# Optimization experiments

Hardware: AMD Instinct MI355X
Metric: run time of the kernel (lower is better)

## Reference

```python
import jax, jax.numpy as jnp
import numpy as np

B, N, DIN, DOUT, H = 4, 2048, 256, 256, 4
HD = DOUT // H
NEG_SLOPE = 0.2


def setup_inputs() -> dict:
    key = jax.random.key(0)
    k1, k2, k3, k4, k5 = jax.random.split(key, 5)
    x = jax.random.normal(k1, (B, N, DIN), dtype=jnp.float32)
    adj = jax.random.randint(k2, (B, N, N), 0, 2).astype(jnp.float32)
    # ensure self-loops so every softmax row has at least one valid entry
    adj = jnp.maximum(adj, jnp.eye(N, dtype=jnp.float32)[None])
    # xavier-uniform-ish scales
    w_bound = float(np.sqrt(6.0 / (DIN + DOUT)))
    a_bound = float(np.sqrt(6.0 / (1 + HD)))
    W = jax.random.uniform(k3, (DOUT, DIN), jnp.float32, -w_bound, w_bound)
    a_src = jax.random.uniform(k4, (H, HD), jnp.float32, -a_bound, a_bound)
    a_dst = jax.random.uniform(k5, (H, HD), jnp.float32, -a_bound, a_bound)
    return {"x": x, "adj": adj, "W": W, "a_src": a_src, "a_dst": a_dst}


def reference(x, adj, W, a_src, a_dst):
    b, n, _ = x.shape
    h = (x @ W.T).reshape(b, n, H, HD)                      # [B,N,H,HD]
    s_src = jnp.einsum('bnhd,hd->bnh', h, a_src)            # [B,N,H]
    s_dst = jnp.einsum('bnhd,hd->bnh', h, a_dst)            # [B,N,H]
    # e[b,i,j,h] = leaky_relu(s_src[b,i,h] + s_dst[b,j,h])
    e = jax.nn.leaky_relu(s_src[:, :, None, :] + s_dst[:, None, :, :], NEG_SLOPE)
    e = jnp.where(adj[..., None] == 0, -jnp.inf, e)         # [B,N,N,H]
    alpha = jax.nn.softmax(e, axis=2)                       # softmax over j (dropout is identity at eval)
    out = jnp.einsum('bijh,bjhd->bihd', alpha, h)           # weighted aggregate
    return out.reshape(b, n, DOUT)
```

## Files before the change

### kernel.cpp

```cpp
#include <hip/hip_runtime.h>
#include <math.h>

#define Bb   4
#define Nn   2048
#define Dd   256
#define Hh   4
#define HDd  64
#define BN   (Bb * Nn)

typedef float v4f __attribute__((ext_vector_type(4)));
typedef short v8s __attribute__((ext_vector_type(8)));

__device__ __forceinline__ unsigned rne_bf16(float f) {
    unsigned u = __float_as_uint(f);
    u += 0x7fffu + ((u >> 16) & 1u);
    return u >> 16;
}

__global__ __launch_bounds__(256, 2) void k_gemm(const float* __restrict__ x,
                                                 const float* __restrict__ W,
                                                 const float* __restrict__ a_src,
                                                 const float* __restrict__ a_dst,
                                                 unsigned short* __restrict__ hbf,
                                                 float* __restrict__ ssrc,
                                                 float* __restrict__ sdst) {
    __shared__ __align__(16) unsigned short xs[2][64 * 72];
    __shared__ __align__(16) unsigned short wsm[2][64 * 72];
    __shared__ float asd[128];

    const int tid = threadIdx.x;
    const int m0 = (int)(blockIdx.x >> 2) * 64;
    const int head = (int)blockIdx.x & 3;
    const int n0 = head * 64;
    const int b = m0 >> 11;
    const int i0loc = m0 & 2047;

    if (tid < 128) {
        int sel = tid >> 6, d = tid & 63;
        asd[tid] = sel ? a_dst[n0 + d] : a_src[n0 + d];
    }

    const int wv = tid >> 6, ln = tid & 63, l15 = ln & 15, l4 = ln >> 4;
    const int mh = wv >> 1, nh = wv & 1;
    const int srow = tid >> 2, kq = (tid & 3) * 16;

    v4f acc[2][2];
#pragma unroll
    for (int g = 0; g < 2; ++g)
#pragma unroll
        for (int t = 0; t < 2; ++t) acc[g][t] = (v4f){0.f, 0.f, 0.f, 0.f};

    for (int st = 0; st < 4; ++st) {
        const int k0 = st * 64;
        __syncthreads();
        {
            float xf[16], wf[16];
            const float* xp = x + (size_t)(m0 + srow) * Dd + k0 + kq;
            const float* wp = W + (size_t)(n0 + srow) * Dd + k0 + kq;
#pragma unroll
            for (int q = 0; q < 4; ++q) {
                *(float4*)&xf[q * 4] = *(const float4*)(xp + q * 4);
                *(float4*)&wf[q * 4] = *(const float4*)(wp + q * 4);
            }
            unsigned xh[8], xl[8], wh[8], wl[8];
#pragma unroll
            for (int j = 0; j < 8; ++j) {
                unsigned h0 = rne_bf16(xf[2 * j]), h1 = rne_bf16(xf[2 * j + 1]);
                float l0 = xf[2 * j] - __uint_as_float(h0 << 16);
                float l1 = xf[2 * j + 1] - __uint_as_float(h1 << 16);
                xh[j] = h0 | (h1 << 16);
                xl[j] = rne_bf16(l0) | (rne_bf16(l1) << 16);
                unsigned g0 = rne_bf16(wf[2 * j]), g1 = rne_bf16(wf[2 * j + 1]);
                float m0f = wf[2 * j] - __uint_as_float(g0 << 16);
                float m1f = wf[2 * j + 1] - __uint_as_float(g1 << 16);
                wh[j] = g0 | (g1 << 16);
                wl[j] = rne_bf16(m0f) | (rne_bf16(m1f) << 16);
            }
            *(uint4*)(xs[0] + srow * 72 + kq)     = make_uint4(xh[0], xh[1], xh[2], xh[3]);
            *(uint4*)(xs[0] + srow * 72 + kq + 8) = make_uint4(xh[4], xh[5], xh[6], xh[7]);
            *(uint4*)(xs[1] + srow * 72 + kq)     = make_uint4(xl[0], xl[1], xl[2], xl[3]);
            *(uint4*)(xs[1] + srow * 72 + kq + 8) = make_uint4(xl[4], xl[5], xl[6], xl[7]);
            *(uint4*)(wsm[0] + srow * 72 + kq)     = make_uint4(wh[0], wh[1], wh[2], wh[3]);
            *(uint4*)(wsm[0] + srow * 72 + kq + 8) = make_uint4(wh[4], wh[5], wh[6], wh[7]);
            *(uint4*)(wsm[1] + srow * 72 + kq)     = make_uint4(wl[0], wl[1], wl[2], wl[3]);
            *(uint4*)(wsm[1] + srow * 72 + kq + 8) = make_uint4(wl[4], wl[5], wl[6], wl[7]);
        }
        __syncthreads();
        {
            v8s ah[2][2], al[2][2], bh_[2][2], bl_[2][2];
#pragma unroll
            for (int g = 0; g < 2; ++g)
#pragma unroll
                for (int kh = 0; kh < 2; ++kh) {
                    int ro = (mh * 32 + g * 16 + l15) * 72 + kh * 32 + l4 * 8;
                    ah[g][kh] = *(const v8s*)(xs[0] + ro);
                    al[g][kh] = *(const v8s*)(xs[1] + ro);
                }
#pragma unroll
            for (int t = 0; t < 2; ++t)
#pragma unroll
                for (int kh = 0; kh < 2; ++kh) {
                    int ro = (nh * 32 + t * 16 + l15) * 72 + kh * 32 + l4 * 8;
                    bh_[t][kh] = *(const v8s*)(wsm[0] + ro);
                    bl_[t][kh] = *(const v8s*)(wsm[1] + ro);
                }
#pragma unroll
            for (int g = 0; g < 2; ++g)
#pragma unroll
                for (int t = 0; t < 2; ++t)
#pragma unroll
                    for (int kh = 0; kh < 2; ++kh) {
                        acc[g][t] = __builtin_amdgcn_mfma_f32_16x16x32_bf16(ah[g][kh], bh_[t][kh], acc[g][t], 0, 0, 0);
                        acc[g][t] = __builtin_amdgcn_mfma_f32_16x16x32_bf16(al[g][kh], bh_[t][kh], acc[g][t], 0, 0, 0);
                        acc[g][t] = __builtin_amdgcn_mfma_f32_16x16x32_bf16(ah[g][kh], bl_[t][kh], acc[g][t], 0, 0, 0);
                    }
        }
    }

    __syncthreads();
    float* T = (float*)&xs[0][0];
#pragma unroll
    for (int g = 0; g < 2; ++g)
#pragma unroll
        for (int t = 0; t < 2; ++t)
#pragma unroll
            for (int r = 0; r < 4; ++r) {
                int d = nh * 32 + t * 16 + l15;
                int m = mh * 32 + g * 16 + l4 * 4 + r;
                T[d * 67 + m] = acc[g][t][r];
            }
    __syncthreads();
    if (tid < 128) {
        int m = tid & 63, sel = tid >> 6;
        float s = 0.f;
#pragma unroll
        for (int d = 0; d < 64; ++d) s += T[d * 67 + m] * asd[sel * 64 + d];
        (sel ? sdst : ssrc)[(size_t)head * BN + (size_t)b * Nn + i0loc + m] = s;
        int dloc = tid >> 1, jh = tid & 1;
        const float* row = T + dloc * 67 + jh * 32;
        unsigned pk[16];
#pragma unroll
        for (int jj = 0; jj < 16; ++jj)
            pk[jj] = rne_bf16(row[jj * 2]) | (rne_bf16(row[jj * 2 + 1]) << 16);
        unsigned short* dst = hbf +
            ((size_t)((b * 64 + (i0loc >> 5) + jh) * 256 + head * HDd + dloc)) * 32;
        uint4* d4 = (uint4*)dst;
        d4[0] = make_uint4(pk[0], pk[1], pk[2], pk[3]);
        d4[1] = make_uint4(pk[4], pk[5], pk[6], pk[7]);
        d4[2] = make_uint4(pk[8], pk[9], pk[10], pk[11]);
        d4[3] = make_uint4(pk[12], pk[13], pk[14], pk[15]);
    }
}

__global__ __launch_bounds__(512, 4) void k_aggr(const unsigned short* __restrict__ hbf,
                                                 const float* __restrict__ adj,
                                                 const float* __restrict__ ssrc,
                                                 const float* __restrict__ sdst,
                                                 float* __restrict__ out) {
    __shared__ __align__(16) unsigned short Aw[2][64 * 72];

    const int tid = threadIdx.x;
    const int bid = (int)blockIdx.x;
    const int hp  = (bid >> 3) & 1;
    const int lin = (bid & 7) | ((bid >> 4) << 3);
    const int b  = lin >> 6;
    const int i0 = (lin & 63) * 32;

    const int gi = tid >> 4, jq = tid & 15;
    const int wv = tid >> 6;
    const int hl = wv >> 2, tl = wv & 3;
    const int ln = tid & 63, l15 = ln & 15, l4 = ln >> 4;

    const float ss0 = ssrc[(size_t)(hp * 2 + 0) * BN + (size_t)b * Nn + i0 + gi];
    const float ss1 = ssrc[(size_t)(hp * 2 + 1) * BN + (size_t)b * Nn + i0 + gi];
    const float* adjr = adj + (size_t)b * Nn * Nn + (size_t)(i0 + gi) * Nn;
    const float* sdr0 = sdst + (size_t)(hp * 2 + 0) * BN + (size_t)b * Nn;
    const float* sdr1 = sdst + (size_t)(hp * 2 + 1) * BN + (size_t)b * Nn;

    const unsigned short* hrow = hbf +
        ((size_t)b * 64 * 256 + (size_t)(hp * 128 + hl * 64 + tl * 16 + l15)) * 32 + l4 * 8;

    const v8s ones = {0x3F80, 0x3F80, 0x3F80, 0x3F80, 0x3F80, 0x3F80, 0x3F80, 0x3F80};

    v4f acc[2], zac[2];
#pragma unroll
    for (int g = 0; g < 2; ++g) {
        acc[g] = (v4f){0.f, 0.f, 0.f, 0.f};
        zac[g] = (v4f){0.f, 0.f, 0.f, 0.f};
    }

    float4 ajv = *(const float4*)(adjr + jq * 4);
    float4 sda = *(const float4*)(sdr0 + jq * 4);
    float4 sdb = *(const float4*)(sdr1 + jq * 4);

    for (int st = 0; st < 32; ++st) {
        {
            const float adjv[4] = {ajv.x, ajv.y, ajv.z, ajv.w};
            const float sa[4] = {sda.x, sda.y, sda.z, sda.w};
            const float sb[4] = {sdb.x, sdb.y, sdb.z, sdb.w};
            unsigned pk0[2], pk1[2];
#pragma unroll
            for (int k = 0; k < 4; ++k) {
                float e0 = ss0 + sa[k];
                float e1 = ss1 + sb[k];
                e0 = fmaxf(e0, 0.2f * e0);
                e1 = fmaxf(e1, 0.2f * e1);
                unsigned u0 = rne_bf16(adjv[k] * __expf(e0));
                unsigned u1 = rne_bf16(adjv[k] * __expf(e1));
                if (k & 1) { pk0[k >> 1] |= u0 << 16; pk1[k >> 1] |= u1 << 16; }
                else       { pk0[k >> 1] = u0;        pk1[k >> 1] = u1; }
            }
            *(uint2*)(Aw[st & 1] + gi * 72 + jq * 4)        = make_uint2(pk0[0], pk0[1]);
            *(uint2*)(Aw[st & 1] + (32 + gi) * 72 + jq * 4) = make_uint2(pk1[0], pk1[1]);
        }
        __syncthreads();
        {
            const int jn = ((st + 1) & 31) * 64;
            ajv = *(const float4*)(adjr + jn + jq * 4);
            sda = *(const float4*)(sdr0 + jn + jq * 4);
            sdb = *(const float4*)(sdr1 + jn + jq * 4);
        }
        {
            const unsigned short* awp = Aw[st & 1];
            v8s b0 = *(const v8s*)(hrow + (size_t)(2 * st + 0) * 8192);
            v8s b1 = *(const v8s*)(hrow + (size_t)(2 * st + 1) * 8192);
            v8s a00 = *(const v8s*)(awp + (hl * 32 + l15) * 72 + l4 * 8);
            v8s a01 = *(const v8s*)(awp + (hl * 32 + l15) * 72 + 32 + l4 * 8);
            v8s a10 = *(const v8s*)(awp + (hl * 32 + 16 + l15) * 72 + l4 * 8);
            v8s a11 = *(const v8s*)(awp + (hl * 32 + 16 + l15) * 72 + 32 + l4 * 8);
            acc[0] = __builtin_amdgcn_mfma_f32_16x16x32_bf16(a00, b0, acc[0], 0, 0, 0);
            acc[0] = __builtin_amdgcn_mfma_f32_16x16x32_bf16(a01, b1, acc[0], 0, 0, 0);
            acc[1] = __builtin_amdgcn_mfma_f32_16x16x32_bf16(a10, b0, acc[1], 0, 0, 0);
            acc[1] = __builtin_amdgcn_mfma_f32_16x16x32_bf16(a11, b1, acc[1], 0, 0, 0);
            zac[0] = __builtin_amdgcn_mfma_f32_16x16x32_bf16(a00, ones, zac[0], 0, 0, 0);
            zac[0] = __builtin_amdgcn_mfma_f32_16x16x32_bf16(a01, ones, zac[0], 0, 0, 0);
            zac[1] = __builtin_amdgcn_mfma_f32_16x16x32_bf16(a10, ones, zac[1], 0, 0, 0);
            zac[1] = __builtin_amdgcn_mfma_f32_16x16x32_bf16(a11, ones, zac[1], 0, 0, 0);
        }
    }

    const int head = hp * 2 + hl;
    const int d = head * HDd + tl * 16 + l15;
#pragma unroll
    for (int g = 0; g < 2; ++g)
#pragma unroll
        for (int r = 0; r < 4; ++r) {
            float zinv = 1.f / zac[g][r];
            int i = i0 + g * 16 + l4 * 4 + r;
            out[((size_t)b * Nn + i) * Dd + d] = acc[g][r] * zinv;
        }
}

extern "C" void kernel_launch(void* const* d_in, const int* in_sizes, int n_in,
                              void* d_out, int out_size, void* d_ws, size_t ws_size,
                              hipStream_t stream) {
    const float* x     = (const float*)d_in[0];
    const float* adj   = (const float*)d_in[1];
    const float* W     = (const float*)d_in[2];
    const float* a_src = (const float*)d_in[3];
    const float* a_dst = (const float*)d_in[4];
    float* out = (float*)d_out;

    unsigned short* hbf = (unsigned short*)d_ws;
    float* ssrc = (float*)(hbf + (size_t)Bb * Nn * Dd);
    float* sdst = ssrc + (size_t)Hh * BN;

    k_gemm<<<dim3(512), dim3(256), 0, stream>>>(x, W, a_src, a_dst, hbf, ssrc, sdst);
    k_aggr<<<dim3(512), dim3(512), 0, stream>>>(hbf, adj, ssrc, sdst, out);
}
```

Baseline: 155.4 us.

## Build attention weights in registers per wave, removing LDS staging and barriers

The aggregation kernel is restructured so each wave owns one head and 16 rows. It computes the bf16 attention weights directly in the MFMA A-operand register layout, so the LDS buffer and per-step __syncthreads are gone. It also issues 4 output-column MFMAs plus one row-sum MFMA per step and software-prefetches adj/sdst two steps ahead and h one step ahead. Scores are pre-scaled by log2(e) so exp2 can replace expf. In exchange, each wave now reads adj rows separately per head (4x adj traffic across waves within a block, though those reads can hit cache), and the block is smaller with more registers per thread.

```diff
diff --git a/kernel.cpp b/kernel.cpp
--- a/kernel.cpp
+++ b/kernel.cpp
@@ -135,7 +135,8 @@
         float s = 0.f;
 #pragma unroll
         for (int d = 0; d < 64; ++d) s += T[d * 67 + m] * asd[sel * 64 + d];
-        (sel ? sdst : ssrc)[(size_t)head * BN + (size_t)b * Nn + i0loc + m] = s;
+        (sel ? sdst : ssrc)[(size_t)head * BN + (size_t)b * Nn + i0loc + m] =
+            s * 1.4426950408889634f;
         int dloc = tid >> 1, jh = tid & 1;
         const float* row = T + dloc * 67 + jh * 32;
         unsigned pk[16];
@@ -152,103 +153,85 @@
     }
 }
 
-__global__ __launch_bounds__(512, 4) void k_aggr(const unsigned short* __restrict__ hbf,
+__global__ __launch_bounds__(256, 2) void k_aggr(const unsigned short* __restrict__ hbf,
                                                  const float* __restrict__ adj,
                                                  const float* __restrict__ ssrc,
                                                  const float* __restrict__ sdst,
                                                  float* __restrict__ out) {
-    __shared__ __align__(16) unsigned short Aw[2][64 * 72];
-
     const int tid = threadIdx.x;
+    const int h = tid >> 6;
     const int bid = (int)blockIdx.x;
-    const int hp  = (bid >> 3) & 1;
-    const int lin = (bid & 7) | ((bid >> 4) << 3);
-    const int b  = lin >> 6;
-    const int i0 = (lin & 63) * 32;
-
-    const int gi = tid >> 4, jq = tid & 15;
-    const int wv = tid >> 6;
-    const int hl = wv >> 2, tl = wv & 3;
+    const int b = bid >> 7;
+    const int i0 = (bid & 127) * 16;
     const int ln = tid & 63, l15 = ln & 15, l4 = ln >> 4;
 
-    const float ss0 = ssrc[(size_t)(hp * 2 + 0) * BN + (size_t)b * Nn + i0 + gi];
-    const float ss1 = ssrc[(size_t)(hp * 2 + 1) * BN + (size_t)b * Nn + i0 + gi];
-    const float* adjr = adj + (size_t)b * Nn * Nn + (size_t)(i0 + gi) * Nn;
-    const float* sdr0 = sdst + (size_t)(hp * 2 + 0) * BN + (size_t)b * Nn;
-    const float* sdr1 = sdst + (size_t)(hp * 2 + 1) * BN + (size_t)b * Nn;
-
+    const float ssv = ssrc[(size_t)h * BN + (size_t)b * Nn + i0 + l15];
+    const float* adjr = adj + (size_t)b * Nn * Nn + (size_t)(i0 + l15) * Nn + l4 * 8;
+    const float* sdr  = sdst + (size_t)h * BN + (size_t)b * Nn + l4 * 8;
     const unsigned short* hrow = hbf +
-        ((size_t)b * 64 * 256 + (size_t)(hp * 128 + hl * 64 + tl * 16 + l15)) * 32 + l4 * 8;
+        ((size_t)(b * 64) * 256 + (size_t)(h * HDd + l15)) * 32 + l4 * 8;
 
     const v8s ones = {0x3F80, 0x3F80, 0x3F80, 0x3F80, 0x3F80, 0x3F80, 0x3F80, 0x3F80};
 
-    v4f acc[2], zac[2];
-#pragma unroll
-    for (int g = 0; g < 2; ++g) {
-        acc[g] = (v4f){0.f, 0.f, 0.f, 0.f};
-        zac[g] = (v4f){0.f, 0.f, 0.f, 0.f};
-    }
-
-    float4 ajv = *(const float4*)(adjr + jq * 4);
-    float4 sda = *(const float4*)(sdr0 + jq * 4);
-    float4 sdb = *(const float4*)(sdr1 + jq * 4);
-
-    for (int st = 0; st < 32; ++st) {
+    v4f acc[4], zac;
+#pragma unroll
+    for (int q = 0; q < 4; ++q) acc[q] = (v4f){0.f, 0.f, 0.f, 0.f};
+    zac = (v4f){0.f, 0.f, 0.f, 0.f};
+
+    float4 aja[2], ajb[2], sda[2], sdb[2];
+    aja[0] = *(const float4*)(adjr);      ajb[0] = *(const float4*)(adjr + 4);
+    sda[0] = *(const float4*)(sdr);       sdb[0] = *(const float4*)(sdr + 4);
+    aja[1] = *(const float4*)(adjr + 32); ajb[1] = *(const float4*)(adjr + 36);
+    sda[1] = *(const float4*)(sdr + 32);  sdb[1] = *(const float4*)(sdr + 36);
+    v8s bfr[4];
+#pragma unroll
+    for (int q = 0; q < 4; ++q) bfr[q] = *(const v8s*)(hrow + q * 512);
+
+#pragma unroll 2
+    for (int st = 0; st < 64; ++st) {
+        const int cur = st & 1;
+        union { v8s v; unsigned u[4]; } A;
         {
-            const float adjv[4] = {ajv.x, ajv.y, ajv.z, ajv.w};
-            const float sa[4] = {sda.x, sda.y, sda.z, sda.w};
-            const float sb[4] = {sdb.x, sdb.y, sdb.z, sdb.w};
-            unsigned pk0[2], pk1[2];
-#pragma unroll
-            for (int k = 0; k < 4; ++k) {
-                float e0 = ss0 + sa[k];
-                float e1 = ss1 + sb[k];
-                e0 = fmaxf(e0, 0.2f * e0);
-                e1 = fmaxf(e1, 0.2f * e1);
-                unsigned u0 = rne_bf16(adjv[k] * __expf(e0));
-                unsigned u1 = rne_bf16(adjv[k] * __expf(e1));
-                if (k & 1) { pk0[k >> 1] |= u0 << 16; pk1[k >> 1] |= u1 << 16; }
-                else       { pk0[k >> 1] = u0;        pk1[k >> 1] = u1; }
-            }
-            *(uint2*)(Aw[st & 1] + gi * 72 + jq * 4)        = make_uint2(pk0[0], pk0[1]);
-            *(uint2*)(Aw[st & 1] + (32 + gi) * 72 + jq * 4) = make_uint2(pk1[0], pk1[1]);
-        }
-        __syncthreads();
-        {
-            const int jn = ((st + 1) & 31) * 64;
-            ajv = *(const float4*)(adjr + jn + jq * 4);
-            sda = *(const float4*)(sdr0 + jn + jq * 4);
-            sdb = *(const float4*)(sdr1 + jn + jq * 4);
-        }
-        {
-            const unsigned short* awp = Aw[st & 1];
-            v8s b0 = *(const v8s*)(hrow + (size_t)(2 * st + 0) * 8192);
-            v8s b1 = *(const v8s*)(hrow + (size_t)(2 * st + 1) * 8192);
-            v8s a00 = *(const v8s*)(awp + (hl * 32 + l15) * 72 + l4 * 8);
-            v8s a01 = *(const v8s*)(awp + (hl * 32 + l15) * 72 + 32 + l4 * 8);
-            v8s a10 = *(const v8s*)(awp + (hl * 32 + 16 + l15) * 72 + l4 * 8);
-            v8s a11 = *(const v8s*)(awp + (hl * 32 + 16 + l15) * 72 + 32 + l4 * 8);
-            acc[0] = __builtin_amdgcn_mfma_f32_16x16x32_bf16(a00, b0, acc[0], 0, 0, 0);
-            acc[0] = __builtin_amdgcn_mfma_f32_16x16x32_bf16(a01, b1, acc[0], 0, 0, 0);
-            acc[1] = __builtin_amdgcn_mfma_f32_16x16x32_bf16(a10, b0, acc[1], 0, 0, 0);
-            acc[1] = __builtin_amdgcn_mfma_f32_16x16x32_bf16(a11, b1, acc[1], 0, 0, 0);
-            zac[0] = __builtin_amdgcn_mfma_f32_16x16x32_bf16(a00, ones, zac[0], 0, 0, 0);
-            zac[0] = __builtin_amdgcn_mfma_f32_16x16x32_bf16(a01, ones, zac[0], 0, 0, 0);
-            zac[1] = __builtin_amdgcn_mfma_f32_16x16x32_bf16(a10, ones, zac[1], 0, 0, 0);
-            zac[1] = __builtin_amdgcn_mfma_f32_16x16x32_bf16(a11, ones, zac[1], 0, 0, 0);
-        }
-    }
-
-    const int head = hp * 2 + hl;
-    const int d = head * HDd + tl * 16 + l15;
-#pragma unroll
-    for (int g = 0; g < 2; ++g)
-#pragma unroll
-        for (int r = 0; r < 4; ++r) {
-            float zinv = 1.f / zac[g][r];
-            int i = i0 + g * 16 + l4 * 4 + r;
-            out[((size_t)b * Nn + i) * Dd + d] = acc[g][r] * zinv;
-        }
+            const float aj8[8] = {aja[cur].x, aja[cur].y, aja[cur].z, aja[cur].w,
+                                  ajb[cur].x, ajb[cur].y, ajb[cur].z, ajb[cur].w};
+            const float sd8[8] = {sda[cur].x, sda[cur].y, sda[cur].z, sda[cur].w,
+                                  sdb[cur].x, sdb[cur].y, sdb[cur].z, sdb[cur].w};
+            unsigned uu[8];
+#pragma unroll
+            for (int jj = 0; jj < 8; ++jj) {
+                float e = ssv + sd8[jj];
+                e = fmaxf(e, 0.2f * e);
+                uu[jj] = rne_bf16(aj8[jj] * __builtin_amdgcn_exp2f(e));
+            }
+#pragma unroll
+            for (int p = 0; p < 4; ++p) A.u[p] = uu[2 * p] | (uu[2 * p + 1] << 16);
+        }
+        v8s b0 = bfr[0], b1 = bfr[1], b2 = bfr[2], b3 = bfr[3];
+        const int s1 = (st + 1) & 63, s2 = (st + 2) & 63;
+#pragma unroll
+        for (int q = 0; q < 4; ++q)
+            bfr[q] = *(const v8s*)(hrow + (size_t)s1 * 8192 + q * 512);
+        aja[cur] = *(const float4*)(adjr + s2 * 32);
+        ajb[cur] = *(const float4*)(adjr + s2 * 32 + 4);
+        sda[cur] = *(const float4*)(sdr + s2 * 32);
+        sdb[cur] = *(const float4*)(sdr + s2 * 32 + 4);
+        acc[0] = __builtin_amdgcn_mfma_f32_16x16x32_bf16(A.v, b0, acc[0], 0, 0, 0);
+        acc[1] = __builtin_amdgcn_mfma_f32_16x16x32_bf16(A.v, b1, acc[1], 0, 0, 0);
+        acc[2] = __builtin_amdgcn_mfma_f32_16x16x32_bf16(A.v, b2, acc[2], 0, 0, 0);
+        acc[3] = __builtin_amdgcn_mfma_f32_16x16x32_bf16(A.v, b3, acc[3], 0, 0, 0);
+        zac    = __builtin_amdgcn_mfma_f32_16x16x32_bf16(A.v, ones, zac, 0, 0, 0);
+    }
+
+#pragma unroll
+    for (int r = 0; r < 4; ++r) {
+        float zinv = 1.f / zac[r];
+        int i = i0 + l4 * 4 + r;
+#pragma unroll
+        for (int q = 0; q < 4; ++q) {
+            int d = h * HDd + q * 16 + l15;
+            out[((size_t)b * Nn + i) * Dd + d] = acc[q][r] * zinv;
+        }
+    }
 }
 
 extern "C" void kernel_launch(void* const* d_in, const int* in_sizes, int n_in,
@@ -266,5 +249,5 @@
     float* sdst = ssrc + (size_t)Hh * BN;
 
     k_gemm<<<dim3(512), dim3(256), 0, stream>>>(x, W, a_src, a_dst, hbf, ssrc, sdst);
-    k_aggr<<<dim3(512), dim3(512), 0, stream>>>(hbf, adj, ssrc, sdst, out);
-}
+    k_aggr<<<dim3(512), dim3(256), 0, stream>>>(hbf, adj, ssrc, sdst, out);
+}
```

Measured after the change: 172.3 us. 1.11x slower.
